# Kernel optimization log

Measured on AMD Instinct MI355X. Metric: run time of the kernel, lower is better.

Reference implementation:

```python
import jax, jax.numpy as jnp
import numpy as np

N = 50000      # nodes
E = 600000     # edges
F_IN = 128     # input features
H = 128        # hidden
C = 40         # classes


def _glorot(key, shape):
    lim = float(np.sqrt(6.0 / (shape[0] + shape[1])))
    return jax.random.uniform(key, shape, jnp.float32, -lim, lim)


def setup_inputs() -> dict:
    key = jax.random.key(0)
    ks = jax.random.split(key, 16)
    inp = {
        "x": jax.random.normal(ks[0], (N, F_IN), jnp.float32),
        "edge_index": jax.random.randint(ks[1], (2, E), 0, N, jnp.int64),
    }
    # SAGEConv params: Wl (neighbor branch, with bias), Wr (root branch), stored [in, out]
    dims = [(F_IN, H), (H, H), (H, H)]
    for i, (din, dout) in enumerate(dims, start=1):
        inp[f"Wl{i}"] = _glorot(ks[2 * i], (din, dout))
        inp[f"bl{i}"] = jnp.zeros((dout,), jnp.float32)
        inp[f"Wr{i}"] = _glorot(ks[2 * i + 1], (din, dout))
    inp["W_lin1"] = _glorot(ks[10], (H, H))
    inp["b_lin1"] = jnp.zeros((H,), jnp.float32)
    inp["W_lin2"] = _glorot(ks[11], (H, C))
    inp["b_lin2"] = jnp.zeros((C,), jnp.float32)
    return inp


def _sage_conv(x, src, dst, Wl, bl, Wr):
    # mean-aggregate neighbor features at destination nodes
    msgs = x[src]  # [E, d] gather
    agg = jax.ops.segment_sum(msgs, dst, num_segments=N)
    deg = jax.ops.segment_sum(jnp.ones((E,), x.dtype), dst, num_segments=N)
    agg = agg / jnp.clip(deg, 1.0)[:, None]
    return agg @ Wl + bl + x @ Wr


def reference(x, edge_index, Wl1, bl1, Wr1, Wl2, bl2, Wr2, Wl3, bl3, Wr3,
              W_lin1, b_lin1, W_lin2, b_lin2):
    src, dst = edge_index[0], edge_index[1]
    h = jax.nn.relu(_sage_conv(x, src, dst, Wl1, bl1, Wr1))
    h = jax.nn.relu(_sage_conv(h, src, dst, Wl2, bl2, Wr2))
    h = jax.nn.relu(_sage_conv(h, src, dst, Wl3, bl3, Wr3))
    h = jax.nn.relu(h @ W_lin1 + b_lin1)
    # dropout: inference mode (training=False) -> identity
    logits = h @ W_lin2 + b_lin2
    return jax.nn.log_softmax(logits, axis=-1)
```

## Files before the change

### kernel.cpp

```cpp
#include <hip/hip_runtime.h>
#include <hip/hip_bf16.h>
#include <math.h>

#define NNODES 50000
#define NEDGES 600000
#define FDIM   128
#define NCLS   40
#define SLOTS  64
#define CVT_BLOCKS 6250
#define PACK_BLOCKS 62
#define CZ_BLOCKS 196
#define PREP_TOTAL (CVT_BLOCKS + PACK_BLOCKS + CZ_BLOCKS)
#define NT16 (NNODES / 16)

typedef __hip_bfloat16 bf16;
typedef short bf16x8 __attribute__((ext_vector_type(8)));
typedef short bf16x4 __attribute__((ext_vector_type(4)));
typedef float f32x4  __attribute__((ext_vector_type(4)));

__device__ __forceinline__ float b2f(short u) {
    union { unsigned int i; float f; } cv;
    cv.i = ((unsigned int)(unsigned short)u) << 16;
    return cv.f;
}
__device__ __forceinline__ short f2b(float f) {
    bf16 h = __float2bfloat16(f);
    return *(const short*)&h;
}
__device__ __forceinline__ float ldf(const void* p, int fp32, int idx) {
    return fp32 ? ((const float*)p)[idx]
                : __bfloat162float(((const bf16*)p)[idx]);
}
__device__ __forceinline__ int wave_is_fp32(const unsigned* p, int lane) {
    unsigned w = p[lane];
    unsigned e = (w >> 7) & 0xFFu;
    int inr = (e >= 100u && e <= 140u) ? 1 : 0;
    return (int)__popcll(__ballot(inr)) < 32;
}
__device__ __forceinline__ int lidx(int row, int col) {
    return row * 128 + ((((col >> 3) ^ (row & 15)) << 3) | (col & 7));
}

__global__ void k_prep(const void* __restrict__ xin,
                       const void* Wl1, const void* Wr1, const void* Wl2,
                       const void* Wr2, const void* Wl3, const void* Wr3,
                       const void* Wlin1, const void* Wlin2,
                       const void* b1, const void* b2, const void* b3,
                       const void* b4, const void* b5,
                       int* __restrict__ cursor, bf16* __restrict__ xb,
                       bf16x8* __restrict__ packed, float* __restrict__ biasf) {
    int b = blockIdx.x, tid = threadIdx.x, lane = tid & 63;
    if (b < CVT_BLOCKS) {
        int xf = wave_is_fp32((const unsigned*)xin, lane);
        int i = b * 256 + tid;
        if (xf) {
            float4 v = ((const float4*)xin)[i];
            bf16x4 o;
            o[0] = f2b(v.x); o[1] = f2b(v.y); o[2] = f2b(v.z); o[3] = f2b(v.w);
            ((bf16x4*)xb)[i] = o;
        } else {
            ((uint2*)xb)[i] = ((const uint2*)xin)[i];
        }
        return;
    }
    if (b >= CVT_BLOCKS + PACK_BLOCKS) {
        int i = (b - CVT_BLOCKS - PACK_BLOCKS) * 256 + tid;
        if (i < NNODES) cursor[i] = 0;
        return;
    }
    int wf = wave_is_fp32((const unsigned*)Wl1, lane);
    int lb = b - CVT_BLOCKS;
    if (lb >= 59) {
        int t = (lb - 59) * 256 + tid;
        if (t >= 5 * 128) return;
        int which = t >> 7, idx = t & 127;
        const void* srcs[5] = {b1, b2, b3, b4, b5};
        int n = (which == 4) ? NCLS : 128;
        float v = 0.f;
        if (idx < n) v = ldf(srcs[which], wf, idx);
        biasf[t] = v;
        return;
    }
    int t2 = lb * 256 + tid;
    int frag = t2 >> 6;
    if (frag >= 236) return;
    int q = lane >> 4, l16 = lane & 15;
    const void* W;
    int kbase, n, ldw = 128, nvalid = 128;
    if (frag < 192) {
        int g = frag >> 6, local = frag & 63;
        int kt = local >> 3, nt = local & 7;
        const void* Wl = (g == 0) ? Wl1 : (g == 1) ? Wl2 : Wl3;
        const void* Wr = (g == 0) ? Wr1 : (g == 1) ? Wr2 : Wr3;
        W = (kt < 4) ? Wl : Wr;
        kbase = (kt & 3) * 32;
        n = nt * 16 + l16;
    } else if (frag < 224) {
        int local = frag - 192;
        int kt = local >> 3, nt = local & 7;
        W = Wlin1; kbase = kt * 32; n = nt * 16 + l16;
    } else {
        int local = frag - 224;
        int kt = local / 3, nt = local % 3;
        W = Wlin2; kbase = kt * 32; n = nt * 16 + l16;
        ldw = NCLS; nvalid = NCLS;
    }
    bf16x8 v;
#pragma unroll
    for (int j = 0; j < 8; j++) {
        float e = 0.f;
        if (n < nvalid) e = ldf(W, wf, (kbase + q * 8 + j) * ldw + n);
        v[j] = f2b(e);
    }
    packed[frag * 64 + lane] = v;
}

__global__ void k_fill(const int* __restrict__ e32, const long long* __restrict__ e64,
                       int* __restrict__ cursor, int* __restrict__ edge_src) {
    int lane = threadIdx.x & 63;
    unsigned hw = ((const unsigned*)e32)[2 * lane + 1];
    int is64 = (__ballot(hw != 0u) == 0ull) ? 1 : 0;
    int i = blockIdx.x * 256 + threadIdx.x;
    if (i >= NEDGES) return;
    int srcn = is64 ? (int)e64[i] : e32[i];
    int dstn = is64 ? (int)e64[NEDGES + i] : e32[NEDGES + i];
    int pos = atomicAdd(&cursor[dstn], 1);
    if (pos < SLOTS) edge_src[dstn * SLOTS + pos] = srcn;
}

__device__ __forceinline__ void agg16(const bf16* __restrict__ x,
        const int* __restrict__ deg, const int* __restrict__ es,
        short* __restrict__ lds, int node0, int lane) {
    const int g = lane >> 4, c = lane & 15;
    const int gsel = lane & 48;
#pragma unroll
    for (int p = 0; p < 4; p++) {
        const int node = node0 + p * 4 + g;
        const int dg = deg[node];
        int ei = es[node * SLOTS + c];
        if ((unsigned)ei >= NNODES) ei = 0;
        float acc[8];
#pragma unroll
        for (int e = 0; e < 8; e++) acc[e] = 0.f;
#pragma unroll
        for (int j = 0; j < 16; j++) {
            int idx = __shfl(ei, gsel | j);
            float m = (j < dg) ? 1.f : 0.f;
            bf16x8 v = *(const bf16x8*)(x + (unsigned)(idx * FDIM + c * 8));
#pragma unroll
            for (int e = 0; e < 8; e++) acc[e] = fmaf(b2f(v[e]), m, acc[e]);
        }
        if (__ballot(dg > 16) != 0ull) {
            for (int jb = 16; jb < SLOTS && __ballot(dg > jb) != 0ull; jb += 16) {
                int ei2 = es[node * SLOTS + jb + c];
                if ((unsigned)ei2 >= NNODES) ei2 = 0;
                for (int j = 0; j < 16; j++) {
                    int idx = __shfl(ei2, gsel | j);
                    float m = (jb + j < dg) ? 1.f : 0.f;
                    bf16x8 v = *(const bf16x8*)(x + (unsigned)(idx * FDIM + c * 8));
#pragma unroll
                    for (int e = 0; e < 8; e++) acc[e] = fmaf(b2f(v[e]), m, acc[e]);
                }
            }
        }
        float inv = (dg > 0) ? 1.f / (float)dg : 0.f;
        bf16x8 o;
#pragma unroll
        for (int e = 0; e < 8; e++) o[e] = f2b(acc[e] * inv);
        *(bf16x8*)(lds + lidx(p * 4 + g, c * 8)) = o;
    }
}

__device__ __forceinline__ void gemm16(int rowbase, int lane,
        short* __restrict__ lds, const bf16* __restrict__ xroot,
        const bf16x8* __restrict__ packed, const float* __restrict__ bias) {
    const int q = lane >> 4, l16 = lane & 15;
    f32x4 acc[8];
#pragma unroll
    for (int n = 0; n < 8; n++) acc[n] = (f32x4){0.f, 0.f, 0.f, 0.f};
#pragma unroll
    for (int kt = 0; kt < 8; kt++) {
        bf16x8 a;
        if (kt < 4)
            a = *(const bf16x8*)(lds + lidx(l16, kt * 32 + q * 8));
        else
            a = *(const bf16x8*)(xroot +
                    (unsigned)((rowbase + l16) * FDIM + (kt - 4) * 32 + q * 8));
#pragma unroll
        for (int n = 0; n < 8; n++)
            acc[n] = __builtin_amdgcn_mfma_f32_16x16x32_bf16(
                a, packed[(kt * 8 + n) * 64 + lane], acc[n], 0, 0, 0);
    }
#pragma unroll
    for (int n = 0; n < 8; n++) {
        int col = n * 16 + l16;
        float bv = bias[col];
#pragma unroll
        for (int r = 0; r < 4; r++)
            lds[lidx(q * 4 + r, col)] = f2b(fmaxf(acc[n][r] + bv, 0.f));
    }
}

__device__ __forceinline__ void store16(int rowbase, int lane,
        const short* __restrict__ lds, bf16* __restrict__ out) {
    const int g = lane >> 4, c = lane & 15;
#pragma unroll
    for (int p = 0; p < 4; p++) {
        bf16x8 v = *(const bf16x8*)(lds + lidx(p * 4 + g, c * 8));
        *(bf16x8*)(out + (unsigned)((rowbase + p * 4 + g) * FDIM + c * 8)) = v;
    }
}

__device__ __forceinline__ void head16(int rowbase, int lane,
        const short* __restrict__ h3, short* __restrict__ h1,
        const bf16x8* __restrict__ packed, const float* __restrict__ bias1,
        const float* __restrict__ bias2, float* __restrict__ out) {
    const int q = lane >> 4, l16 = lane & 15;
    f32x4 acc[8];
#pragma unroll
    for (int n = 0; n < 8; n++) acc[n] = (f32x4){0.f, 0.f, 0.f, 0.f};
#pragma unroll
    for (int kt = 0; kt < 4; kt++) {
        bf16x8 a = *(const bf16x8*)(h3 + lidx(l16, kt * 32 + q * 8));
#pragma unroll
        for (int n = 0; n < 8; n++)
            acc[n] = __builtin_amdgcn_mfma_f32_16x16x32_bf16(
                a, packed[(192 + kt * 8 + n) * 64 + lane], acc[n], 0, 0, 0);
    }
#pragma unroll
    for (int n = 0; n < 8; n++) {
        int col = n * 16 + l16;
        float bv = bias1[col];
#pragma unroll
        for (int r = 0; r < 4; r++)
            h1[lidx(q * 4 + r, col)] = f2b(fmaxf(acc[n][r] + bv, 0.f));
    }
    f32x4 acc2[3];
#pragma unroll
    for (int n = 0; n < 3; n++) acc2[n] = (f32x4){0.f, 0.f, 0.f, 0.f};
#pragma unroll
    for (int kt = 0; kt < 4; kt++) {
        bf16x8 a = *(const bf16x8*)(h1 + lidx(l16, kt * 32 + q * 8));
#pragma unroll
        for (int n = 0; n < 3; n++)
            acc2[n] = __builtin_amdgcn_mfma_f32_16x16x32_bf16(
                a, packed[(224 + kt * 3 + n) * 64 + lane], acc2[n], 0, 0, 0);
    }
    const float NEG = -1e30f;
    bool v2ok = (l16 < 8);
#pragma unroll
    for (int r = 0; r < 4; r++) {
        unsigned row = (unsigned)(rowbase + q * 4 + r);
        float v0 = acc2[0][r] + bias2[l16];
        float v1 = acc2[1][r] + bias2[16 + l16];
        float v2 = v2ok ? (acc2[2][r] + bias2[32 + l16]) : NEG;
        float m = fmaxf(fmaxf(v0, v1), v2);
#pragma unroll
        for (int mk = 1; mk < 16; mk <<= 1) m = fmaxf(m, __shfl_xor(m, mk));
        float sden = expf(v0 - m) + expf(v1 - m) + (v2ok ? expf(v2 - m) : 0.f);
#pragma unroll
        for (int mk = 1; mk < 16; mk <<= 1) sden += __shfl_xor(sden, mk);
        float l = m + logf(sden);
        out[row * NCLS + l16] = v0 - l;
        out[row * NCLS + 16 + l16] = v1 - l;
        if (v2ok) out[row * NCLS + 32 + l16] = v2 - l;
    }
}

__global__ void __launch_bounds__(64)
k_layer(const bf16* __restrict__ src, const int* __restrict__ deg,
        const int* __restrict__ edge_src, const bf16x8* __restrict__ packed,
        const float* __restrict__ bias, bf16* __restrict__ out) {
    __shared__ __align__(16) short lds[16 * 128];
    const int lane = threadIdx.x;
    const int rowbase = blockIdx.x * 16;
    agg16(src, deg, edge_src, lds, rowbase, lane);
    gemm16(rowbase, lane, lds, src, packed, bias);
    store16(rowbase, lane, lds, out);
}

__global__ void __launch_bounds__(64)
k_layer3head(const bf16* __restrict__ src, const int* __restrict__ deg,
             const int* __restrict__ edge_src, const bf16x8* __restrict__ packed,
             const float* __restrict__ biasf, float* __restrict__ out) {
    __shared__ __align__(16) short h3[16 * 128];
    __shared__ __align__(16) short h1[16 * 128];
    const int lane = threadIdx.x;
    const int rowbase = blockIdx.x * 16;
    agg16(src, deg, edge_src, h3, rowbase, lane);
    gemm16(rowbase, lane, h3, src, packed + 128 * 64, biasf + 256);
    head16(rowbase, lane, h3, h1, packed, biasf + 384, biasf + 512, out);
}

extern "C" void kernel_launch(void* const* d_in, const int* in_sizes, int n_in,
                              void* d_out, int out_size, void* d_ws, size_t ws_size,
                              hipStream_t stream) {
    char* ws = (char*)d_ws;
    size_t off = 0;
    auto take = [&](size_t bytes) {
        void* pp = ws + off;
        off = (off + bytes + 255) & ~(size_t)255;
        return pp;
    };
    const int* e32 = (const int*)d_in[1];
    const long long* e64 = (const long long*)d_in[1];
    int* cursor    = (int*)take(NNODES * 4);
    int* edge_src  = (int*)take((size_t)NNODES * SLOTS * 4);
    bf16x8* packed = (bf16x8*)take(236 * 64 * 16);
    float* biasf   = (float*)take(5 * 128 * 4);
    bf16* xb       = (bf16*)take((size_t)NNODES * FDIM * 2);
    bf16* bufA     = (bf16*)take((size_t)NNODES * FDIM * 2);
    float* outp    = (float*)d_out;
    bf16* bufB     = xb;

    k_prep<<<PREP_TOTAL, 256, 0, stream>>>(
        d_in[0], d_in[2], d_in[4], d_in[5], d_in[7], d_in[8], d_in[10],
        d_in[11], d_in[13], d_in[3], d_in[6], d_in[9], d_in[12], d_in[14],
        cursor, xb, packed, biasf);
    k_fill<<<(NEDGES + 255) / 256, 256, 0, stream>>>(e32, e64, cursor, edge_src);

    k_layer<<<NT16, 64, 0, stream>>>(xb, cursor, edge_src, packed, biasf, bufA);
    k_layer<<<NT16, 64, 0, stream>>>(bufA, cursor, edge_src,
                                     packed + 64 * 64, biasf + 128, bufB);
    k_layer3head<<<NT16, 64, 0, stream>>>(bufB, cursor, edge_src,
                                          packed, biasf, outp);
}
```

Measured before the change: 238.2 us.

## Fuse edge fill into prep kernel, prefetch root rows, pack bf16 accumulation

Splits cursor zeroing into a small vectorised kernel and merges the edge-bucketing fill into the prep kernel, so feature conversion and weight packing run in the same launch as the fill, with each fill thread handling two edges. The layer kernels load the root-feature A fragments into registers before aggregation, and agg16 hoists the degree and edge-index loads out of the per-node loop. The bf16-to-float unpack now uses shift/mask on 32-bit words with packed float2 multiply-adds. A dead, unused k_all kernel with a stray label and a bogus store is left in the file, and register pressure in the layer kernels rises.

```diff
diff --git a/kernel.cpp b/kernel.cpp
--- a/kernel.cpp
+++ b/kernel.cpp
@@ -7,20 +7,22 @@
 #define FDIM   128
 #define NCLS   40
 #define SLOTS  64
+#define FILL_BLOCKS 1172
 #define CVT_BLOCKS 6250
 #define PACK_BLOCKS 62
-#define CZ_BLOCKS 196
-#define PREP_TOTAL (CVT_BLOCKS + PACK_BLOCKS + CZ_BLOCKS)
+#define ALL_TOTAL (FILL_BLOCKS + CVT_BLOCKS + PACK_BLOCKS)
 #define NT16 (NNODES / 16)
 
 typedef __hip_bfloat16 bf16;
 typedef short bf16x8 __attribute__((ext_vector_type(8)));
 typedef short bf16x4 __attribute__((ext_vector_type(4)));
 typedef float f32x4  __attribute__((ext_vector_type(4)));
-
-__device__ __forceinline__ float b2f(short u) {
-    union { unsigned int i; float f; } cv;
-    cv.i = ((unsigned int)(unsigned short)u) << 16;
+typedef float f32x2  __attribute__((ext_vector_type(2)));
+typedef unsigned u32x4 __attribute__((ext_vector_type(4)));
+
+__device__ __forceinline__ float u2f(unsigned u) {
+    union { unsigned i; float f; } cv;
+    cv.i = u;
     return cv.f;
 }
 __device__ __forceinline__ short f2b(float f) {
@@ -41,18 +43,70 @@
     return row * 128 + ((((col >> 3) ^ (row & 15)) << 3) | (col & 7));
 }
 
-__global__ void k_prep(const void* __restrict__ xin,
+__global__ void k_zero(int* __restrict__ cursor) {
+    int i = blockIdx.x * 256 + threadIdx.x;
+    if (i < NNODES / 4) ((int4*)cursor)[i] = (int4){0, 0, 0, 0};
+}
+
+__global__ void k_all(const int* __restrict__ e32, const long long* __restrict__ e64,
+                      const void* __restrict__ xin,
+                      const void* Wl1, const void* Wr1, const void* Wl2,
+                      const void* Wr2, const void* Wl3, const void* Wr3,
+                      const void* Wlin1, const void* Wlin2,
+                      const void* b1, const void* b2, const void* b3,
+                      const void* b4, const void* b5,
+                      int* __restrict__ cursor, bf16* __restrict__ xb,
+                      bf16x8* __restrict__ packed, float* __restrict__ biasf) {
+    int b = blockIdx.x, tid = threadIdx.x, lane = tid & 63;
+    if (b < FILL_BLOCKS) {
+        unsigned hw = ((const unsigned*)e32)[2 * lane + 1];
+        int is64 = (__ballot(hw != 0u) == 0ull) ? 1 : 0;
+        int i0 = b * 512 + tid;
+        int i1 = i0 + 256;
+        if (i0 < NEDGES) {
+            int srcn = is64 ? (int)e64[i0] : e32[i0];
+            int dstn = is64 ? (int)e64[NEDGES + i0] : e32[NEDGES + i0];
+            int pos = atomicAdd(&cursor[dstn], 1);
+            if (pos < SLOTS) edge_src_store: ;
+            if (pos < SLOTS) ((int*)packed - 0)[0] = 0;
+        }
+        return;
+    }
+    return;
+}
+
+__global__ void k_all2(const int* __restrict__ e32, const long long* __restrict__ e64,
+                       const void* __restrict__ xin,
                        const void* Wl1, const void* Wr1, const void* Wl2,
                        const void* Wr2, const void* Wl3, const void* Wr3,
                        const void* Wlin1, const void* Wlin2,
                        const void* b1, const void* b2, const void* b3,
                        const void* b4, const void* b5,
-                       int* __restrict__ cursor, bf16* __restrict__ xb,
+                       int* __restrict__ cursor, int* __restrict__ edge_src,
+                       bf16* __restrict__ xb,
                        bf16x8* __restrict__ packed, float* __restrict__ biasf) {
     int b = blockIdx.x, tid = threadIdx.x, lane = tid & 63;
-    if (b < CVT_BLOCKS) {
+    if (b < FILL_BLOCKS) {
+        unsigned hw = ((const unsigned*)e32)[2 * lane + 1];
+        int is64 = (__ballot(hw != 0u) == 0ull) ? 1 : 0;
+        int i0 = b * 512 + tid;
+        int i1 = i0 + 256;
+        int s0 = 0, d0 = 0, s1 = 0, d1 = 0;
+        bool v0 = i0 < NEDGES, v1 = i1 < NEDGES;
+        if (v0) { s0 = is64 ? (int)e64[i0] : e32[i0];
+                  d0 = is64 ? (int)e64[NEDGES + i0] : e32[NEDGES + i0]; }
+        if (v1) { s1 = is64 ? (int)e64[i1] : e32[i1];
+                  d1 = is64 ? (int)e64[NEDGES + i1] : e32[NEDGES + i1]; }
+        int p0 = 0, p1 = 0;
+        if (v0) p0 = atomicAdd(&cursor[d0], 1);
+        if (v1) p1 = atomicAdd(&cursor[d1], 1);
+        if (v0 && p0 < SLOTS) edge_src[d0 * SLOTS + p0] = s0;
+        if (v1 && p1 < SLOTS) edge_src[d1 * SLOTS + p1] = s1;
+        return;
+    }
+    if (b < FILL_BLOCKS + CVT_BLOCKS) {
         int xf = wave_is_fp32((const unsigned*)xin, lane);
-        int i = b * 256 + tid;
+        int i = (b - FILL_BLOCKS) * 256 + tid;
         if (xf) {
             float4 v = ((const float4*)xin)[i];
             bf16x4 o;
@@ -63,13 +117,8 @@
         }
         return;
     }
-    if (b >= CVT_BLOCKS + PACK_BLOCKS) {
-        int i = (b - CVT_BLOCKS - PACK_BLOCKS) * 256 + tid;
-        if (i < NNODES) cursor[i] = 0;
-        return;
-    }
     int wf = wave_is_fp32((const unsigned*)Wl1, lane);
-    int lb = b - CVT_BLOCKS;
+    int lb = b - FILL_BLOCKS - CVT_BLOCKS;
     if (lb >= 59) {
         int t = (lb - 59) * 256 + tid;
         if (t >= 5 * 128) return;
@@ -115,65 +164,68 @@
     packed[frag * 64 + lane] = v;
 }
 
-__global__ void k_fill(const int* __restrict__ e32, const long long* __restrict__ e64,
-                       int* __restrict__ cursor, int* __restrict__ edge_src) {
-    int lane = threadIdx.x & 63;
-    unsigned hw = ((const unsigned*)e32)[2 * lane + 1];
-    int is64 = (__ballot(hw != 0u) == 0ull) ? 1 : 0;
-    int i = blockIdx.x * 256 + threadIdx.x;
-    if (i >= NEDGES) return;
-    int srcn = is64 ? (int)e64[i] : e32[i];
-    int dstn = is64 ? (int)e64[NEDGES + i] : e32[NEDGES + i];
-    int pos = atomicAdd(&cursor[dstn], 1);
-    if (pos < SLOTS) edge_src[dstn * SLOTS + pos] = srcn;
-}
-
 __device__ __forceinline__ void agg16(const bf16* __restrict__ x,
         const int* __restrict__ deg, const int* __restrict__ es,
         short* __restrict__ lds, int node0, int lane) {
     const int g = lane >> 4, c = lane & 15;
     const int gsel = lane & 48;
+    int dgp[4], eip[4];
+#pragma unroll
+    for (int p = 0; p < 4; p++) dgp[p] = deg[node0 + p * 4 + g];
 #pragma unroll
     for (int p = 0; p < 4; p++) {
-        const int node = node0 + p * 4 + g;
-        const int dg = deg[node];
-        int ei = es[node * SLOTS + c];
-        if ((unsigned)ei >= NNODES) ei = 0;
-        float acc[8];
-#pragma unroll
-        for (int e = 0; e < 8; e++) acc[e] = 0.f;
+        int ei = es[(node0 + p * 4 + g) * SLOTS + c];
+        eip[p] = ((unsigned)ei >= NNODES) ? 0 : ei;
+    }
+#pragma unroll
+    for (int p = 0; p < 4; p++) {
+        const int dg = dgp[p];
+        f32x2 acc2[4];
+#pragma unroll
+        for (int k = 0; k < 4; k++) acc2[k] = (f32x2){0.f, 0.f};
 #pragma unroll
         for (int j = 0; j < 16; j++) {
-            int idx = __shfl(ei, gsel | j);
+            int idx = __shfl(eip[p], gsel | j);
             float m = (j < dg) ? 1.f : 0.f;
-            bf16x8 v = *(const bf16x8*)(x + (unsigned)(idx * FDIM + c * 8));
-#pragma unroll
-            for (int e = 0; e < 8; e++) acc[e] = fmaf(b2f(v[e]), m, acc[e]);
+            f32x2 m2 = (f32x2){m, m};
+            u32x4 u = *(const u32x4*)(x + (unsigned)(idx * FDIM + c * 8));
+#pragma unroll
+            for (int k = 0; k < 4; k++) {
+                f32x2 vv = (f32x2){u2f(u[k] << 16), u2f(u[k] & 0xFFFF0000u)};
+                acc2[k] += vv * m2;
+            }
         }
         if (__ballot(dg > 16) != 0ull) {
             for (int jb = 16; jb < SLOTS && __ballot(dg > jb) != 0ull; jb += 16) {
-                int ei2 = es[node * SLOTS + jb + c];
+                int ei2 = es[(node0 + p * 4 + g) * SLOTS + jb + c];
                 if ((unsigned)ei2 >= NNODES) ei2 = 0;
                 for (int j = 0; j < 16; j++) {
                     int idx = __shfl(ei2, gsel | j);
                     float m = (jb + j < dg) ? 1.f : 0.f;
-                    bf16x8 v = *(const bf16x8*)(x + (unsigned)(idx * FDIM + c * 8));
-#pragma unroll
-                    for (int e = 0; e < 8; e++) acc[e] = fmaf(b2f(v[e]), m, acc[e]);
+                    f32x2 m2 = (f32x2){m, m};
+                    u32x4 u = *(const u32x4*)(x + (unsigned)(idx * FDIM + c * 8));
+#pragma unroll
+                    for (int k = 0; k < 4; k++) {
+                        f32x2 vv = (f32x2){u2f(u[k] << 16), u2f(u[k] & 0xFFFF0000u)};
+                        acc2[k] += vv * m2;
+                    }
                 }
             }
         }
         float inv = (dg > 0) ? 1.f / (float)dg : 0.f;
         bf16x8 o;
 #pragma unroll
-        for (int e = 0; e < 8; e++) o[e] = f2b(acc[e] * inv);
+        for (int k = 0; k < 4; k++) {
+            o[2 * k]     = f2b(acc2[k].x * inv);
+            o[2 * k + 1] = f2b(acc2[k].y * inv);
+        }
         *(bf16x8*)(lds + lidx(p * 4 + g, c * 8)) = o;
     }
 }
 
-__device__ __forceinline__ void gemm16(int rowbase, int lane,
-        short* __restrict__ lds, const bf16* __restrict__ xroot,
-        const bf16x8* __restrict__ packed, const float* __restrict__ bias) {
+__device__ __forceinline__ void gemm16(int lane, short* __restrict__ lds,
+        const bf16x8 rt[4], const bf16x8* __restrict__ packed,
+        const float* __restrict__ bias) {
     const int q = lane >> 4, l16 = lane & 15;
     f32x4 acc[8];
 #pragma unroll
@@ -184,8 +236,7 @@
         if (kt < 4)
             a = *(const bf16x8*)(lds + lidx(l16, kt * 32 + q * 8));
         else
-            a = *(const bf16x8*)(xroot +
-                    (unsigned)((rowbase + l16) * FDIM + (kt - 4) * 32 + q * 8));
+            a = rt[kt - 4];
 #pragma unroll
         for (int n = 0; n < 8; n++)
             acc[n] = __builtin_amdgcn_mfma_f32_16x16x32_bf16(
@@ -274,8 +325,14 @@
     __shared__ __align__(16) short lds[16 * 128];
     const int lane = threadIdx.x;
     const int rowbase = blockIdx.x * 16;
+    const int q = lane >> 4, l16 = lane & 15;
+    bf16x8 rt[4];
+#pragma unroll
+    for (int kt = 0; kt < 4; kt++)
+        rt[kt] = *(const bf16x8*)(src +
+                     (unsigned)((rowbase + l16) * FDIM + kt * 32 + q * 8));
     agg16(src, deg, edge_src, lds, rowbase, lane);
-    gemm16(rowbase, lane, lds, src, packed, bias);
+    gemm16(lane, lds, rt, packed, bias);
     store16(rowbase, lane, lds, out);
 }
 
@@ -287,8 +344,14 @@
     __shared__ __align__(16) short h1[16 * 128];
     const int lane = threadIdx.x;
     const int rowbase = blockIdx.x * 16;
+    const int q = lane >> 4, l16 = lane & 15;
+    bf16x8 rt[4];
+#pragma unroll
+    for (int kt = 0; kt < 4; kt++)
+        rt[kt] = *(const bf16x8*)(src +
+                     (unsigned)((rowbase + l16) * FDIM + kt * 32 + q * 8));
     agg16(src, deg, edge_src, h3, rowbase, lane);
-    gemm16(rowbase, lane, h3, src, packed + 128 * 64, biasf + 256);
+    gemm16(lane, h3, rt, packed + 128 * 64, biasf + 256);
     head16(rowbase, lane, h3, h1, packed, biasf + 384, biasf + 512, out);
 }
 
@@ -313,11 +376,11 @@
     float* outp    = (float*)d_out;
     bf16* bufB     = xb;
 
-    k_prep<<<PREP_TOTAL, 256, 0, stream>>>(
-        d_in[0], d_in[2], d_in[4], d_in[5], d_in[7], d_in[8], d_in[10],
-        d_in[11], d_in[13], d_in[3], d_in[6], d_in[9], d_in[12], d_in[14],
-        cursor, xb, packed, biasf);
-    k_fill<<<(NEDGES + 255) / 256, 256, 0, stream>>>(e32, e64, cursor, edge_src);
+    k_zero<<<49, 256, 0, stream>>>(cursor);
+    k_all2<<<ALL_TOTAL, 256, 0, stream>>>(
+        e32, e64, d_in[0], d_in[2], d_in[4], d_in[5], d_in[7], d_in[8],
+        d_in[10], d_in[11], d_in[13], d_in[3], d_in[6], d_in[9], d_in[12],
+        d_in[14], cursor, edge_src, xb, packed, biasf);
 
     k_layer<<<NT16, 64, 0, stream>>>(xb, cursor, edge_src, packed, biasf, bufA);
     k_layer<<<NT16, 64, 0, stream>>>(bufA, cursor, edge_src,
```

New measurement: 239.6 us. Within noise of the previous version (+0.6%).
